# Performance work log

Measured on AMD Instinct MI355X. Metric: run time of the kernel, lower is better.

## Reference

```python
import jax, jax.numpy as jnp
import numpy as np

B, L, H, K = 16, 2048, 1024, 4  # batch, seq, hidden, heads
NEG = -1e9  # stand-in for -inf in masked softmax (grad-safe, prob ~0)

def setup_inputs() -> dict:
    key = jax.random.key(0)
    ks = jax.random.split(key, 6)
    s = 0.02
    hidden = jax.random.normal(ks[0], (B, L, H), dtype=jnp.float32)
    masks = jax.random.randint(ks[1], (B, L), 0, 2).astype(jnp.bool_)
    Wp = jax.random.normal(ks[2], (H, H * K), dtype=jnp.float32) * s
    W1 = jax.random.normal(ks[3], (K, H, H // 2), dtype=jnp.float32) * s
    b1 = jax.random.normal(ks[4], (K, H // 2), dtype=jnp.float32) * s
    W2 = jax.random.normal(ks[5], (K, H // 2), dtype=jnp.float32) * s
    return {"hidden": hidden, "masks": masks, "Wp": Wp, "W1": W1, "b1": b1, "W2": W2}

def reference(hidden, masks, Wp, W1, b1, W2):
    b, l, h = hidden.shape
    k = W1.shape[0]
    # projection (no bias), split into heads: [b,l,k,h]
    proj = (hidden @ Wp).reshape(b, l, k, h)
    # per-head tanh MLP score: Linear(h, h//2)+bias -> tanh -> Linear(h//2, 1)
    a1 = jnp.tanh(jnp.einsum('blkh,khd->blkd', proj, W1) + b1)  # [b,l,k,h//2]
    logits = jnp.einsum('blkd,kd->kbl', a1, W2)                 # [k,b,l]
    # masked softmax over sequence dim
    logits = jnp.where(masks[None, :, :], NEG, logits)
    attn = jax.nn.softmax(logits, axis=-1)                      # [k,b,l]
    return attn
```

## Files before the change

### kernel.cpp

```cpp
#include <hip/hip_runtime.h>
#include <hip/hip_bf16.h>
#include <cstdint>
#include <cstddef>

#define HD   1024
#define NK   4
#define DD   512
#define LSEQ 2048
#define NB   16
#define MTOT (NB*LSEQ)
#define NF2  (NK*DD)

typedef __attribute__((ext_vector_type(4))) float f32x4;
typedef __attribute__((ext_vector_type(8))) short bf16x8;

#define GLOAD16(gp, lp) __builtin_amdgcn_global_load_lds( \
    (const __attribute__((address_space(1))) void*)(gp),  \
    (__attribute__((address_space(3))) void*)(lp), 16, 0, 0)

static __device__ __forceinline__ ushort f2bf(float f) {
  union { float f; unsigned u; } x; x.f = f;
  unsigned r = x.u + 0x7FFFu + ((x.u >> 16) & 1u);
  return (ushort)(r >> 16);
}

static __device__ __forceinline__ unsigned pkbf(float a, float b) {
  float2 t; t.x = a; t.y = b;
  __hip_bfloat162 h = __float22bfloat162_rn(t);
  return *reinterpret_cast<unsigned*>(&h);
}

static __device__ __forceinline__ float fast_tanh(float x) {
  x = fminf(fmaxf(x, -15.f), 15.f);
  float t = __expf(2.0f * x);
  return (t - 1.0f) / (t + 1.0f);
}

__global__ void detect_mask_kernel(const unsigned char* __restrict__ m, int nbytes,
                                   int* __restrict__ flag) {
  int found = 0;
  for (int i = blockIdx.x * blockDim.x + threadIdx.x; i < nbytes;
       i += gridDim.x * blockDim.x)
    if ((i & 3) && m[i]) found = 1;
  if (__any(found) && (threadIdx.x & 63) == 0) atomicOr(flag, 1);
}

__global__ void cvt_wp_heads_kernel(const float* __restrict__ Wp,
                                    ushort* __restrict__ WpH) {
  long i4 = ((long)blockIdx.x * blockDim.x + threadIdx.x) * 4;
  int h = (int)(i4 >> 20);
  int c = (int)((i4 >> 10) & 1023);
  int j = (int)(i4 & 1023);
  f32x4 v = *(const f32x4*)(Wp + (long)c * (NK * HD) + h * HD + j);
  ushort4 o; o.x = f2bf(v.x); o.y = f2bf(v.y); o.z = f2bf(v.z); o.w = f2bf(v.w);
  *(ushort4*)(WpH + i4) = o;
}

__global__ void transpose_cvt_kernel(const float* __restrict__ src,
                                     ushort* __restrict__ dst,
                                     int R, int C, long sBatch, long dBatch) {
  __shared__ float tile[32][33];
  const float* s = src + blockIdx.z * sBatch;
  ushort* d = dst + blockIdx.z * dBatch;
  int c0 = blockIdx.x * 32, r0 = blockIdx.y * 32;
  int tx = threadIdx.x, ty = threadIdx.y;
  #pragma unroll
  for (int i = 0; i < 32; i += 8)
    tile[ty + i][tx] = s[(long)(r0 + ty + i) * C + (c0 + tx)];
  __syncthreads();
  #pragma unroll
  for (int i = 0; i < 32; i += 8)
    d[(long)(c0 + ty + i) * R + (r0 + tx)] = f2bf(tile[tx][ty + i]);
}

template<int MODE, int AF32>
__global__ __launch_bounds__(256, 2)
void gemm128_kernel(const void* __restrict__ A, int lda, long aZs,
                    const ushort* __restrict__ Bt, int ldb, long bZs, int Kdim,
                    ushort* __restrict__ Cout, int ldc, long cZs,
                    const float* __restrict__ b1, const float* __restrict__ W2,
                    float* __restrict__ partialOut, int m0glob) {
  __shared__ __align__(16) char lds[AF32 ? 24576 : 16384];
  constexpr int AB = AF32 ? 16384 : 8192;

  const int tid = threadIdx.x;
  const int wave = tid >> 6, lane = tid & 63;
  const int z = blockIdx.z;

  const int bid = blockIdx.x + gridDim.x * blockIdx.y;
  const int nMB = gridDim.x, nNB = gridDim.y;
  int m0, n0;
  if ((nMB & 7) == 0) {
    const int x = bid & 7, j = bid >> 3;
    m0 = (x * (nMB >> 3) + j / nNB) * 128;
    n0 = (j % nNB) * 128;
  } else {
    m0 = (bid % nMB) * 128; n0 = (bid / nMB) * 128;
  }

  const float*  Agf = (const float*)A  + z * aZs + (long)m0 * lda;
  const ushort* Agb = (const ushort*)A + z * aZs + (long)m0 * lda;
  const ushort* Bg  = Bt + z * bZs + (long)n0 * ldb;

  const int wr = wave >> 1, wc = wave & 1;
  const int rsel = lane & 15, ch = lane >> 4;

  const int chunkC = (ch ^ ((rsel >> 1) & 3)) << 4;
  const int laneB = AB + wc * 4096 + rsel * 64 + chunkC;
  const int sA = rsel & 7;
  const int laneA0 = (wr * 64 + rsel) * 128 + (((ch * 2)     ^ sA) << 4);
  const int laneA1 = (wr * 64 + rsel) * 128 + (((ch * 2 + 1) ^ sA) << 4);
  const int laneAb = wr * 4096 + rsel * 64 + chunkC;

  const int stRowA = wave * 8 + (lane >> 3);
  const int cSrcA = (((lane & 7) ^ ((lane >> 3) & 7))) * 4;
  const int stRowB = wave * 16 + (lane >> 2);
  const int stCg = ((lane & 3) ^ ((lane >> 3) & 3)) * 8;

  f32x4 acc[4][4] = {};

  const int ksteps = Kdim >> 5;
  for (int kt = 0; kt < ksteps; ++kt) {
    if constexpr (AF32) {
      const int kk32 = (kt << 5) + cSrcA;
      #pragma unroll
      for (int i = 0; i < 4; ++i)
        GLOAD16(Agf + (long)(i * 32 + stRowA) * lda + kk32,
                (char*)lds + i * 4096 + wave * 1024);
      const int kkb = (kt << 5) + stCg;
      GLOAD16(Bg + (long)stRowB * ldb + kkb,        (char*)lds + AB + wave * 1024);
      GLOAD16(Bg + (long)(64 + stRowB) * ldb + kkb, (char*)lds + AB + 4096 + wave * 1024);
    } else {
      const int kk = (kt << 5) + stCg;
      GLOAD16(Agb + (long)stRowB * lda + kk,        (char*)lds + wave * 1024);
      GLOAD16(Agb + (long)(64 + stRowB) * lda + kk, (char*)lds + 4096 + wave * 1024);
      GLOAD16(Bg + (long)stRowB * ldb + kk,         (char*)lds + AB + wave * 1024);
      GLOAD16(Bg + (long)(64 + stRowB) * ldb + kk,  (char*)lds + AB + 4096 + wave * 1024);
    }
    __syncthreads();

    bf16x8 aF[4], bF[4];
    if constexpr (AF32) {
      #pragma unroll
      for (int mf = 0; mf < 4; ++mf) {
        f32x4 va = *(const f32x4*)(lds + laneA0 + mf * 2048);
        f32x4 vb = *(const f32x4*)(lds + laneA1 + mf * 2048);
        unsigned* ap = (unsigned*)&aF[mf];
        ap[0] = pkbf(va[0], va[1]); ap[1] = pkbf(va[2], va[3]);
        ap[2] = pkbf(vb[0], vb[1]); ap[3] = pkbf(vb[2], vb[3]);
      }
    } else {
      #pragma unroll
      for (int mf = 0; mf < 4; ++mf)
        aF[mf] = *(const bf16x8*)(lds + laneAb + mf * 1024);
    }
    #pragma unroll
    for (int nf = 0; nf < 4; ++nf)
      bF[nf] = *(const bf16x8*)(lds + laneB + nf * 1024);
    #pragma unroll
    for (int mf = 0; mf < 4; ++mf)
      #pragma unroll
      for (int nf = 0; nf < 4; ++nf)
        acc[mf][nf] = __builtin_amdgcn_mfma_f32_16x16x32_bf16(
            aF[mf], bF[nf], acc[mf][nf], 0, 0, 0);
    __syncthreads();
  }

  if constexpr (MODE == 0) {
    #pragma unroll
    for (int mf = 0; mf < 4; ++mf)
      #pragma unroll
      for (int nf = 0; nf < 4; ++nf) {
        const int col = n0 + wc * 64 + nf * 16 + (lane & 15);
        #pragma unroll
        for (int r = 0; r < 4; ++r) {
          const int row = m0 + wr * 64 + mf * 16 + ((lane >> 4) << 2) + r;
          Cout[z * cZs + (long)row * ldc + col] = f2bf(acc[mf][nf][r]);
        }
      }
  } else {
    float b1v[4], w2v[4];
    #pragma unroll
    for (int nf = 0; nf < 4; ++nf) {
      const int col = n0 + wc * 64 + nf * 16 + (lane & 15);
      b1v[nf] = b1[col];
      w2v[nf] = W2[col];
    }
    const int wslice = (n0 + wc * 64) >> 6;
    float* pb = partialOut + (long)wslice * MTOT + m0glob + m0 + wr * 64;
    #pragma unroll
    for (int mf = 0; mf < 4; ++mf)
      #pragma unroll
      for (int r = 0; r < 4; ++r) {
        float s = 0.f;
        #pragma unroll
        for (int nf = 0; nf < 4; ++nf)
          s += fast_tanh(acc[mf][nf][r] + b1v[nf]) * w2v[nf];
        s += __shfl_xor(s, 1, 64);
        s += __shfl_xor(s, 2, 64);
        s += __shfl_xor(s, 4, 64);
        s += __shfl_xor(s, 8, 64);
        if ((lane & 15) == 0)
          pb[mf * 16 + ((lane >> 4) << 2) + r] = s;
      }
  }
}

__global__ __launch_bounds__(256)
void masked_softmax_kernel(const float* __restrict__ partial,
                           const unsigned char* __restrict__ maskB,
                           const int* __restrict__ maskI,
                           const int* __restrict__ flag,
                           float* __restrict__ out) {
  const int kb = blockIdx.x;
  const int k = kb >> 4, b = kb & (NB - 1);
  const long base = (long)kb * LSEQ;
  const bool isByte = (*flag != 0);
  const int tid = threadIdx.x;
  const float* pk = partial + (long)(k * 8) * MTOT + (long)b * LSEQ;

  float x[8];
  float mx = -3.0e38f;
  #pragma unroll
  for (int j = 0; j < 8; ++j) {
    int l = tid + j * 256;
    float v = 0.f;
    #pragma unroll
    for (int ws = 0; ws < 8; ++ws) v += pk[(long)ws * MTOT + l];
    bool msk = isByte ? (maskB[b * LSEQ + l] != 0) : (maskI[b * LSEQ + l] != 0);
    v = msk ? -1e9f : v;
    x[j] = v; mx = fmaxf(mx, v);
  }
  __shared__ float redm[4], reds[4];
  #pragma unroll
  for (int off = 32; off >= 1; off >>= 1) mx = fmaxf(mx, __shfl_xor(mx, off, 64));
  if ((tid & 63) == 0) redm[tid >> 6] = mx;
  __syncthreads();
  mx = fmaxf(fmaxf(redm[0], redm[1]), fmaxf(redm[2], redm[3]));

  float sum = 0.f;
  #pragma unroll
  for (int j = 0; j < 8; ++j) { x[j] = __expf(x[j] - mx); sum += x[j]; }
  #pragma unroll
  for (int off = 32; off >= 1; off >>= 1) sum += __shfl_xor(sum, off, 64);
  if ((tid & 63) == 0) reds[tid >> 6] = sum;
  __syncthreads();
  sum = reds[0] + reds[1] + reds[2] + reds[3];

  float inv = 1.0f / sum;
  #pragma unroll
  for (int j = 0; j < 8; ++j) out[base + tid + j * 256] = x[j] * inv;
}

extern "C" void kernel_launch(void* const* d_in, const int* in_sizes, int n_in,
                              void* d_out, int out_size, void* d_ws, size_t ws_size,
                              hipStream_t stream) {
  const float* hidden = (const float*)d_in[0];
  const void*  masks  = d_in[1];
  const float* Wp     = (const float*)d_in[2];
  const float* W1     = (const float*)d_in[3];
  const float* b1     = (const float*)d_in[4];
  const float* W2     = (const float*)d_in[5];
  float* out = (float*)d_out;

  char* ws = (char*)d_ws;
  ushort* W1T      = (ushort*)(ws + 0);
  ushort* WpH      = (ushort*)(ws + 4194304);
  ushort* WfT      = (ushort*)(ws + 12582912);
  float*  partial  = (float*) (ws + 16777216);
  int*    flag     = (int*)   (ws + 20971520);

  hipMemsetAsync(flag, 0, 256, stream);

  detect_mask_kernel<<<8, 256, 0, stream>>>((const unsigned char*)masks, NB * LSEQ, flag);

  dim3 tb(32, 8);
  transpose_cvt_kernel<<<dim3(DD / 32, HD / 32, NK), tb, 0, stream>>>(
      W1, W1T, HD, DD, (long)HD * DD, (long)DD * HD);
  cvt_wp_heads_kernel<<<4096, 256, 0, stream>>>(Wp, WpH);

  gemm128_kernel<0, 0><<<dim3(DD / 128, HD / 128, NK), 256, 0, stream>>>(
      W1T, HD, (long)DD * HD,
      WpH, HD, (long)HD * HD, HD,
      WfT, HD, (long)DD * HD,
      nullptr, nullptr, nullptr, 0);

  gemm128_kernel<1, 1><<<dim3(MTOT / 128, NF2 / 128, 1), 256, 0, stream>>>(
      hidden, HD, 0,
      WfT, HD, 0, HD,
      nullptr, 0, 0,
      b1, W2, partial, 0);

  masked_softmax_kernel<<<NK * NB, 256, 0, stream>>>(
      partial, (const unsigned char*)masks, (const int*)masks, flag, out);
}
```

Measured before the change: 277.4 us.

## Register-prefetch fp32 A tile, convert to bf16 before LDS store

The fp32-A GEMM path no longer stages fp32 A tiles into LDS through direct global-to-LDS loads. Each thread now prefetches the next k-step's fp32 A values into registers one iteration ahead, converts them to bf16 and writes them to LDS itself. This halves the LDS footprint and A-tile LDS traffic and overlaps global A loads with MFMA work, using a hand-placed waitcnt and raw s_barrier instead of __syncthreads. It also hoists the b1/W2 epilogue loads before the main loop, at the cost of more live registers and a fragile manual wait count.

Measured after the change: 258.9 us. 1.07x faster.

```diff
diff --git a/kernel.cpp b/kernel.cpp
--- a/kernel.cpp
+++ b/kernel.cpp
@@ -73,15 +73,14 @@
     d[(long)(c0 + ty + i) * R + (r0 + tx)] = f2bf(tile[tx][ty + i]);
 }
 
-template<int MODE, int AF32>
+template<int MODE, int AF32W>
 __global__ __launch_bounds__(256, 2)
 void gemm128_kernel(const void* __restrict__ A, int lda, long aZs,
                     const ushort* __restrict__ Bt, int ldb, long bZs, int Kdim,
                     ushort* __restrict__ Cout, int ldc, long cZs,
                     const float* __restrict__ b1, const float* __restrict__ W2,
                     float* __restrict__ partialOut, int m0glob) {
-  __shared__ __align__(16) char lds[AF32 ? 24576 : 16384];
-  constexpr int AB = AF32 ? 16384 : 8192;
+  __shared__ __align__(16) char lds[16384];
 
   const int tid = threadIdx.x;
   const int wave = tid >> 6, lane = tid & 63;
@@ -104,56 +103,74 @@
 
   const int wr = wave >> 1, wc = wave & 1;
   const int rsel = lane & 15, ch = lane >> 4;
-
   const int chunkC = (ch ^ ((rsel >> 1) & 3)) << 4;
-  const int laneB = AB + wc * 4096 + rsel * 64 + chunkC;
-  const int sA = rsel & 7;
-  const int laneA0 = (wr * 64 + rsel) * 128 + (((ch * 2)     ^ sA) << 4);
-  const int laneA1 = (wr * 64 + rsel) * 128 + (((ch * 2 + 1) ^ sA) << 4);
-  const int laneAb = wr * 4096 + rsel * 64 + chunkC;
-
-  const int stRowA = wave * 8 + (lane >> 3);
-  const int cSrcA = (((lane & 7) ^ ((lane >> 3) & 7))) * 4;
-  const int stRowB = wave * 16 + (lane >> 2);
+  const int laneA = wr * 4096 + rsel * 64 + chunkC;
+  const int laneB = 8192 + wc * 4096 + rsel * 64 + chunkC;
+
+  const int stRow = wave * 16 + (lane >> 2);
   const int stCg = ((lane & 3) ^ ((lane >> 3) & 3)) * 8;
+  const int ldsOff = wave * 1024;
+
+  float b1v[4], w2v[4];
+  if constexpr (MODE == 1) {
+    #pragma unroll
+    for (int nf = 0; nf < 4; ++nf) {
+      const int col = n0 + wc * 64 + nf * 16 + (lane & 15);
+      b1v[nf] = b1[col];
+      w2v[nf] = W2[col];
+    }
+  }
 
   f32x4 acc[4][4] = {};
-
   const int ksteps = Kdim >> 5;
+
+  f32x4 aR[2][2];
+  if constexpr (AF32W) {
+    #pragma unroll
+    for (int i = 0; i < 2; ++i) {
+      const float* ap = Agf + (long)(i * 64 + stRow) * lda + stCg;
+      aR[i][0] = *(const f32x4*)ap;
+      aR[i][1] = *(const f32x4*)(ap + 4);
+    }
+  }
+
   for (int kt = 0; kt < ksteps; ++kt) {
-    if constexpr (AF32) {
-      const int kk32 = (kt << 5) + cSrcA;
-      #pragma unroll
-      for (int i = 0; i < 4; ++i)
-        GLOAD16(Agf + (long)(i * 32 + stRowA) * lda + kk32,
-                (char*)lds + i * 4096 + wave * 1024);
+    if constexpr (AF32W) {
+      #pragma unroll
+      for (int i = 0; i < 2; ++i) {
+        uint4 o;
+        o.x = pkbf(aR[i][0][0], aR[i][0][1]);
+        o.y = pkbf(aR[i][0][2], aR[i][0][3]);
+        o.z = pkbf(aR[i][1][0], aR[i][1][1]);
+        o.w = pkbf(aR[i][1][2], aR[i][1][3]);
+        *(uint4*)((char*)lds + i * 4096 + ldsOff + lane * 16) = o;
+      }
       const int kkb = (kt << 5) + stCg;
-      GLOAD16(Bg + (long)stRowB * ldb + kkb,        (char*)lds + AB + wave * 1024);
-      GLOAD16(Bg + (long)(64 + stRowB) * ldb + kkb, (char*)lds + AB + 4096 + wave * 1024);
+      GLOAD16(Bg + (long)stRow * ldb + kkb,        (char*)lds + 8192 + ldsOff);
+      GLOAD16(Bg + (long)(64 + stRow) * ldb + kkb, (char*)lds + 12288 + ldsOff);
+      const int ktn = (kt + 1 < ksteps) ? kt + 1 : kt;
+      #pragma unroll
+      for (int i = 0; i < 2; ++i) {
+        const float* ap = Agf + (long)(i * 64 + stRow) * lda + (ktn << 5) + stCg;
+        aR[i][0] = *(const f32x4*)ap;
+        aR[i][1] = *(const f32x4*)(ap + 4);
+      }
+      asm volatile("s_waitcnt vmcnt(4) lgkmcnt(0)" ::: "memory");
+      __builtin_amdgcn_sched_barrier(0);
+      __builtin_amdgcn_s_barrier();
     } else {
       const int kk = (kt << 5) + stCg;
-      GLOAD16(Agb + (long)stRowB * lda + kk,        (char*)lds + wave * 1024);
-      GLOAD16(Agb + (long)(64 + stRowB) * lda + kk, (char*)lds + 4096 + wave * 1024);
-      GLOAD16(Bg + (long)stRowB * ldb + kk,         (char*)lds + AB + wave * 1024);
-      GLOAD16(Bg + (long)(64 + stRowB) * ldb + kk,  (char*)lds + AB + 4096 + wave * 1024);
+      GLOAD16(Agb + (long)stRow * lda + kk,        (char*)lds + ldsOff);
+      GLOAD16(Agb + (long)(64 + stRow) * lda + kk, (char*)lds + 4096 + ldsOff);
+      GLOAD16(Bg + (long)stRow * ldb + kk,         (char*)lds + 8192 + ldsOff);
+      GLOAD16(Bg + (long)(64 + stRow) * ldb + kk,  (char*)lds + 12288 + ldsOff);
+      __syncthreads();
     }
-    __syncthreads();
 
     bf16x8 aF[4], bF[4];
-    if constexpr (AF32) {
-      #pragma unroll
-      for (int mf = 0; mf < 4; ++mf) {
-        f32x4 va = *(const f32x4*)(lds + laneA0 + mf * 2048);
-        f32x4 vb = *(const f32x4*)(lds + laneA1 + mf * 2048);
-        unsigned* ap = (unsigned*)&aF[mf];
-        ap[0] = pkbf(va[0], va[1]); ap[1] = pkbf(va[2], va[3]);
-        ap[2] = pkbf(vb[0], vb[1]); ap[3] = pkbf(vb[2], vb[3]);
-      }
-    } else {
-      #pragma unroll
-      for (int mf = 0; mf < 4; ++mf)
-        aF[mf] = *(const bf16x8*)(lds + laneAb + mf * 1024);
-    }
+    #pragma unroll
+    for (int mf = 0; mf < 4; ++mf)
+      aF[mf] = *(const bf16x8*)(lds + laneA + mf * 1024);
     #pragma unroll
     for (int nf = 0; nf < 4; ++nf)
       bF[nf] = *(const bf16x8*)(lds + laneB + nf * 1024);
@@ -163,7 +180,11 @@
       for (int nf = 0; nf < 4; ++nf)
         acc[mf][nf] = __builtin_amdgcn_mfma_f32_16x16x32_bf16(
             aF[mf], bF[nf], acc[mf][nf], 0, 0, 0);
-    __syncthreads();
+
+    if constexpr (AF32W)
+      __builtin_amdgcn_s_barrier();
+    else
+      __syncthreads();
   }
 
   if constexpr (MODE == 0) {
@@ -179,29 +200,22 @@
         }
       }
   } else {
-    float b1v[4], w2v[4];
-    #pragma unroll
-    for (int nf = 0; nf < 4; ++nf) {
-      const int col = n0 + wc * 64 + nf * 16 + (lane & 15);
-      b1v[nf] = b1[col];
-      w2v[nf] = W2[col];
-    }
     const int wslice = (n0 + wc * 64) >> 6;
     float* pb = partialOut + (long)wslice * MTOT + m0glob + m0 + wr * 64;
     #pragma unroll
     for (int mf = 0; mf < 4; ++mf)
       #pragma unroll
       for (int r = 0; r < 4; ++r) {
-        float s = 0.f;
+        float sv = 0.f;
         #pragma unroll
         for (int nf = 0; nf < 4; ++nf)
-          s += fast_tanh(acc[mf][nf][r] + b1v[nf]) * w2v[nf];
-        s += __shfl_xor(s, 1, 64);
-        s += __shfl_xor(s, 2, 64);
-        s += __shfl_xor(s, 4, 64);
-        s += __shfl_xor(s, 8, 64);
+          sv += fast_tanh(acc[mf][nf][r] + b1v[nf]) * w2v[nf];
+        sv += __shfl_xor(sv, 1, 64);
+        sv += __shfl_xor(sv, 2, 64);
+        sv += __shfl_xor(sv, 4, 64);
+        sv += __shfl_xor(sv, 8, 64);
         if ((lane & 15) == 0)
-          pb[mf * 16 + ((lane >> 4) << 2) + r] = s;
+          pb[mf * 16 + ((lane >> 4) << 2) + r] = sv;
       }
   }
 }
```
